# Performance work log

Hardware: AMD Instinct MI355X
Metric: run time of the kernel (lower is better)

Reference implementation:

```python
import jax, jax.numpy as jnp
from jax import lax
import numpy as np

B, C, H, W = 16, 64, 224, 224
O = 128
PH, PW = 16, 16          # patch_size (== patch_stride => non-overlapping tiling)
CH, CW = 3, 3            # compressor_size
STRIDE = (1, 1)


def setup_inputs() -> dict:
    key = jax.random.key(0)
    k_x, k_w, k_c = jax.random.split(key, 3)
    x = jax.random.normal(k_x, (B, C, H, W), dtype=jnp.float32)
    # xavier-uniform-like init scales
    pw_scale = float(np.sqrt(6.0 / (PH * PW + PH * PW)))
    patch_weight = jax.random.uniform(k_w, (C, PH, PW), jnp.float32, -pw_scale, pw_scale)
    patch_bias = jnp.zeros((C, PH, PW), jnp.float32)
    c_scale = float(np.sqrt(6.0 / (CH * CW + CH * CW)))
    compressor = jax.random.uniform(k_c, (O, CH, CW), jnp.float32, -c_scale, c_scale)
    return {"x": x, "patch_weight": patch_weight, "patch_bias": patch_bias,
            "compressor": compressor}


def _self_conv2d(x, patch_weight, patch_bias, compressor):
    b, c, h, w = x.shape
    # tile into non-overlapping patches: (B, C, nH, PH, nW, PW)
    y = x.reshape(b, c, h // PH, PH, w // PW, PW)
    # per-channel, per-intra-patch-position affine (broadcast over batch & tiles)
    y = y * patch_weight.reshape(1, c, 1, PH, 1, PW) + patch_bias.reshape(1, c, 1, PH, 1, PW)
    y = y.reshape(b, c, h, w)
    # compressor: channel-shared kernel -> (O, C, CH, CW)
    kernel = jnp.broadcast_to(compressor[:, None, :, :], (compressor.shape[0], c, CH, CW))
    out = lax.conv_general_dilated(
        y, kernel, window_strides=STRIDE, padding='VALID',
        dimension_numbers=('NCHW', 'OIHW', 'NCHW'))
    return out  # (B, O, H-CH+1, W-CW+1)


def reference(x, patch_weight, patch_bias, compressor):
    return _self_conv2d(x, patch_weight, patch_bias, compressor)
```

## Files before the change

kernel.cpp:

```cpp
#include <hip/hip_runtime.h>


#define NB 16
#define NC 64
#define NH 224
#define NW 224
#define NO 128
#define OH 222
#define OW 222

__global__ __launch_bounds__(256) void chansum_kernel(
    const float* __restrict__ x, const float* __restrict__ pw,
    const float* __restrict__ pb, float* __restrict__ s)
{
    int q   = blockIdx.x * 256 + threadIdx.x;
    int w4  = q % 56;
    int tmp = q / 56;
    int h   = tmp % NH;
    int b   = tmp / NH;
    int w0  = w4 * 4;
    int hp  = h & 15;
    int wq  = w0 & 15;

    const float4* xp  = (const float4*)(x + (((size_t)b * NC) * NH + h) * NW + w0);
    const float4* pwp = (const float4*)(pw + hp * 16 + wq);
    const float4* pbp = (const float4*)(pb + hp * 16 + wq);

    float4 acc = make_float4(0.f, 0.f, 0.f, 0.f);
    #pragma unroll 8
    for (int c = 0; c < NC; ++c) {
        float4 xv  = xp[(size_t)c * (NH * NW / 4)];
        float4 pwv = pwp[c * 64];
        float4 pbv = pbp[c * 64];
        acc.x = fmaf(xv.x, pwv.x, acc.x) + pbv.x;
        acc.y = fmaf(xv.y, pwv.y, acc.y) + pbv.y;
        acc.z = fmaf(xv.z, pwv.z, acc.z) + pbv.z;
        acc.w = fmaf(xv.w, pwv.w, acc.w) + pbv.w;
    }
    ((float4*)s)[q] = acc;
}

__global__ __launch_bounds__(128) void conv_kernel(
    const float* __restrict__ s, const float* __restrict__ comp,
    float* __restrict__ out)
{
    int bi = blockIdx.x;
    int b  = bi / OH;
    int i  = bi - b * OH;
    int jp = threadIdx.x;
    if (jp >= OW / 2) return;

    float r[3][4];
    #pragma unroll
    for (int kh = 0; kh < 3; ++kh) {
        const float2* sp = (const float2*)(s + (((size_t)b * NH) + i + kh) * NW + 2 * jp);
        float2 lo = sp[0], hi = sp[1];
        r[kh][0] = lo.x; r[kh][1] = lo.y; r[kh][2] = hi.x; r[kh][3] = hi.y;
    }

    float2* outp = (float2*)out + ((size_t)b * NO * OH + i) * (OW / 2) + jp;
    const size_t ostride = (size_t)OH * (OW / 2);

    #pragma unroll 4
    for (int o = 0; o < NO; ++o) {
        const float* cw = comp + o * 9;
        float a0 = 0.f, a1 = 0.f;
        #pragma unroll
        for (int kh = 0; kh < 3; ++kh) {
            float c0 = cw[kh * 3 + 0], c1 = cw[kh * 3 + 1], c2 = cw[kh * 3 + 2];
            a0 = fmaf(r[kh][0], c0, a0);
            a0 = fmaf(r[kh][1], c1, a0);
            a0 = fmaf(r[kh][2], c2, a0);
            a1 = fmaf(r[kh][1], c0, a1);
            a1 = fmaf(r[kh][2], c1, a1);
            a1 = fmaf(r[kh][3], c2, a1);
        }
        outp[(size_t)o * ostride] = make_float2(a0, a1);
    }
}

__global__ __launch_bounds__(128) void fused_kernel(
    const float* __restrict__ x, const float* __restrict__ pw,
    const float* __restrict__ pb, const float* __restrict__ comp,
    float* __restrict__ out)
{
    __shared__ float s[3 * NW];
    int bi = blockIdx.x;
    int b  = bi / OH;
    int i  = bi - b * OH;

    for (int p = threadIdx.x; p < 3 * NW; p += 128) {
        int rr = p / NW, w = p - rr * NW;
        int h  = i + rr;
        int hp = h & 15, wq = w & 15;
        const float* xp  = x + (((size_t)b * NC) * NH + h) * NW + w;
        const float* pwp = pw + hp * 16 + wq;
        const float* pbp = pb + hp * 16 + wq;
        float acc = 0.f;
        for (int c = 0; c < NC; ++c)
            acc = fmaf(xp[(size_t)c * NH * NW], pwp[c * 256], acc) + pbp[c * 256];
        s[p] = acc;
    }
    __syncthreads();

    int jp = threadIdx.x;
    if (jp >= OW / 2) return;

    float r[3][4];
    #pragma unroll
    for (int kh = 0; kh < 3; ++kh)
        #pragma unroll
        for (int m = 0; m < 4; ++m)
            r[kh][m] = s[kh * NW + 2 * jp + m];

    float2* outp = (float2*)out + ((size_t)b * NO * OH + i) * (OW / 2) + jp;
    const size_t ostride = (size_t)OH * (OW / 2);

    #pragma unroll 4
    for (int o = 0; o < NO; ++o) {
        const float* cw = comp + o * 9;
        float a0 = 0.f, a1 = 0.f;
        #pragma unroll
        for (int kh = 0; kh < 3; ++kh) {
            float c0 = cw[kh * 3 + 0], c1 = cw[kh * 3 + 1], c2 = cw[kh * 3 + 2];
            a0 = fmaf(r[kh][0], c0, a0);
            a0 = fmaf(r[kh][1], c1, a0);
            a0 = fmaf(r[kh][2], c2, a0);
            a1 = fmaf(r[kh][1], c0, a1);
            a1 = fmaf(r[kh][2], c1, a1);
            a1 = fmaf(r[kh][3], c2, a1);
        }
        outp[(size_t)o * ostride] = make_float2(a0, a1);
    }
}

extern "C" void kernel_launch(void* const* d_in, const int* in_sizes, int n_in,
                              void* d_out, int out_size, void* d_ws, size_t ws_size,
                              hipStream_t stream) {
    const float* x    = (const float*)d_in[0];
    const float* pw   = (const float*)d_in[1];
    const float* pb   = (const float*)d_in[2];
    const float* comp = (const float*)d_in[3];
    float* out = (float*)d_out;

    const size_t s_bytes = (size_t)NB * NH * NW * sizeof(float);
    if (ws_size >= s_bytes) {
        float* s = (float*)d_ws;
        chansum_kernel<<<(NB * NH * (NW / 4)) / 256, 256, 0, stream>>>(x, pw, pb, s);
        conv_kernel<<<NB * OH, 128, 0, stream>>>(s, comp, out);
    } else {
        fused_kernel<<<NB * OH, 128, 0, stream>>>(x, pw, pb, comp, out);
    }
}
```

Measured before the change: 588.8 us.

## Presum bias, give each thread two rows in chansum, four outputs per thread in conv

Adds a tiny kernel that sums the patch bias over channels once, so the channel-sum kernel no longer loads the bias per channel. The channel-sum kernel now has each thread process two rows 112 apart and reuse one patch-weight load for both. The conv kernel now computes four adjacent outputs per thread from a 3x6 register window and writes them with a packed 16-byte store (8-byte aligned, since the row width 222 is not a multiple of 4), with a two-wide tail at the last column. The aim is fewer weight and bias loads and wider stores, at the cost of an extra kernel launch and lower thread counts in both main kernels.

```diff
diff --git a/kernel.cpp b/kernel.cpp
--- a/kernel.cpp
+++ b/kernel.cpp
@@ -9,73 +9,119 @@
 #define OH 222
 #define OW 222
 
-__global__ __launch_bounds__(256) void chansum_kernel(
+#define S_BYTES ((size_t)NB * NH * NW * sizeof(float))
+
+struct __attribute__((packed, aligned(8))) f4u { float x, y, z, w; };
+
+__global__ __launch_bounds__(256) void biassum_kernel(
+    const float* __restrict__ pb, float* __restrict__ pbsum)
+{
+    int t = threadIdx.x;
+    float a = 0.f;
+    #pragma unroll
+    for (int c = 0; c < NC; ++c) a += pb[c * 256 + t];
+    pbsum[t] = a;
+}
+
+__global__ __launch_bounds__(128) void chansum2_kernel(
     const float* __restrict__ x, const float* __restrict__ pw,
-    const float* __restrict__ pb, float* __restrict__ s)
-{
-    int q   = blockIdx.x * 256 + threadIdx.x;
+    const float* __restrict__ pbsum, float* __restrict__ s)
+{
+    int q   = blockIdx.x * 128 + threadIdx.x;
     int w4  = q % 56;
     int tmp = q / 56;
-    int h   = tmp % NH;
-    int b   = tmp / NH;
+    int h   = tmp % 112;
+    int b   = tmp / 112;
     int w0  = w4 * 4;
     int hp  = h & 15;
     int wq  = w0 & 15;
 
-    const float4* xp  = (const float4*)(x + (((size_t)b * NC) * NH + h) * NW + w0);
+    const float4* xp0 = (const float4*)(x + (((size_t)b * NC) * NH + h) * NW + w0);
+    const float4* xp1 = xp0 + (112 * NW / 4);
     const float4* pwp = (const float4*)(pw + hp * 16 + wq);
-    const float4* pbp = (const float4*)(pb + hp * 16 + wq);
-
-    float4 acc = make_float4(0.f, 0.f, 0.f, 0.f);
+
+    float4 a0 = make_float4(0.f, 0.f, 0.f, 0.f);
+    float4 a1 = make_float4(0.f, 0.f, 0.f, 0.f);
     #pragma unroll 8
     for (int c = 0; c < NC; ++c) {
-        float4 xv  = xp[(size_t)c * (NH * NW / 4)];
-        float4 pwv = pwp[c * 64];
-        float4 pbv = pbp[c * 64];
-        acc.x = fmaf(xv.x, pwv.x, acc.x) + pbv.x;
-        acc.y = fmaf(xv.y, pwv.y, acc.y) + pbv.y;
-        acc.z = fmaf(xv.z, pwv.z, acc.z) + pbv.z;
-        acc.w = fmaf(xv.w, pwv.w, acc.w) + pbv.w;
-    }
-    ((float4*)s)[q] = acc;
-}
-
-__global__ __launch_bounds__(128) void conv_kernel(
+        float4 x0 = xp0[(size_t)c * (NH * NW / 4)];
+        float4 x1 = xp1[(size_t)c * (NH * NW / 4)];
+        float4 wv = pwp[c * 64];
+        a0.x = fmaf(x0.x, wv.x, a0.x);
+        a0.y = fmaf(x0.y, wv.y, a0.y);
+        a0.z = fmaf(x0.z, wv.z, a0.z);
+        a0.w = fmaf(x0.w, wv.w, a0.w);
+        a1.x = fmaf(x1.x, wv.x, a1.x);
+        a1.y = fmaf(x1.y, wv.y, a1.y);
+        a1.z = fmaf(x1.z, wv.z, a1.z);
+        a1.w = fmaf(x1.w, wv.w, a1.w);
+    }
+    float4 bv = *(const float4*)(pbsum + hp * 16 + wq);
+    a0.x += bv.x; a0.y += bv.y; a0.z += bv.z; a0.w += bv.w;
+    a1.x += bv.x; a1.y += bv.y; a1.z += bv.z; a1.w += bv.w;
+
+    size_t so = ((size_t)b * NH + h) * NW + w0;
+    *(float4*)(s + so)                    = a0;
+    *(float4*)(s + so + (size_t)112 * NW) = a1;
+}
+
+__global__ __launch_bounds__(128) void conv2_kernel(
     const float* __restrict__ s, const float* __restrict__ comp,
     float* __restrict__ out)
 {
     int bi = blockIdx.x;
-    int b  = bi / OH;
-    int i  = bi - b * OH;
-    int jp = threadIdx.x;
-    if (jp >= OW / 2) return;
-
-    float r[3][4];
+    int b  = bi / 111;
+    int ig = bi - b * 111;
+    int r  = threadIdx.x >> 6;
+    int jp = threadIdx.x & 63;
+    int i  = 2 * ig + r;
+    if (jp >= 56) return;
+    int j0 = jp * 4;
+
+    float rv[3][6];
     #pragma unroll
     for (int kh = 0; kh < 3; ++kh) {
-        const float2* sp = (const float2*)(s + (((size_t)b * NH) + i + kh) * NW + 2 * jp);
-        float2 lo = sp[0], hi = sp[1];
-        r[kh][0] = lo.x; r[kh][1] = lo.y; r[kh][2] = hi.x; r[kh][3] = hi.y;
-    }
-
-    float2* outp = (float2*)out + ((size_t)b * NO * OH + i) * (OW / 2) + jp;
-    const size_t ostride = (size_t)OH * (OW / 2);
+        const float* sp = s + (((size_t)b * NH) + i + kh) * NW + j0;
+        float4 v = *(const float4*)sp;
+        rv[kh][0] = v.x; rv[kh][1] = v.y; rv[kh][2] = v.z; rv[kh][3] = v.w;
+        if (jp < 55) {
+            float2 t = *(const float2*)(sp + 4);
+            rv[kh][4] = t.x; rv[kh][5] = t.y;
+        } else {
+            rv[kh][4] = 0.f; rv[kh][5] = 0.f;
+        }
+    }
+
+    float* outp = out + ((size_t)b * NO * OH + i) * OW + j0;
+    const size_t ostride = (size_t)OH * OW;
 
     #pragma unroll 4
     for (int o = 0; o < NO; ++o) {
         const float* cw = comp + o * 9;
-        float a0 = 0.f, a1 = 0.f;
+        float a0 = 0.f, a1 = 0.f, a2 = 0.f, a3 = 0.f;
         #pragma unroll
         for (int kh = 0; kh < 3; ++kh) {
             float c0 = cw[kh * 3 + 0], c1 = cw[kh * 3 + 1], c2 = cw[kh * 3 + 2];
-            a0 = fmaf(r[kh][0], c0, a0);
-            a0 = fmaf(r[kh][1], c1, a0);
-            a0 = fmaf(r[kh][2], c2, a0);
-            a1 = fmaf(r[kh][1], c0, a1);
-            a1 = fmaf(r[kh][2], c1, a1);
-            a1 = fmaf(r[kh][3], c2, a1);
-        }
-        outp[(size_t)o * ostride] = make_float2(a0, a1);
+            a0 = fmaf(rv[kh][0], c0, a0);
+            a0 = fmaf(rv[kh][1], c1, a0);
+            a0 = fmaf(rv[kh][2], c2, a0);
+            a1 = fmaf(rv[kh][1], c0, a1);
+            a1 = fmaf(rv[kh][2], c1, a1);
+            a1 = fmaf(rv[kh][3], c2, a1);
+            a2 = fmaf(rv[kh][2], c0, a2);
+            a2 = fmaf(rv[kh][3], c1, a2);
+            a2 = fmaf(rv[kh][4], c2, a2);
+            a3 = fmaf(rv[kh][3], c0, a3);
+            a3 = fmaf(rv[kh][4], c1, a3);
+            a3 = fmaf(rv[kh][5], c2, a3);
+        }
+        float* op = outp + (size_t)o * ostride;
+        if (jp < 55) {
+            f4u v; v.x = a0; v.y = a1; v.z = a2; v.w = a3;
+            *(f4u*)op = v;
+        } else {
+            *(float2*)op = make_float2(a0, a1);
+        }
     }
 }
 
@@ -106,12 +152,12 @@
     int jp = threadIdx.x;
     if (jp >= OW / 2) return;
 
-    float r[3][4];
+    float rr[3][4];
     #pragma unroll
     for (int kh = 0; kh < 3; ++kh)
         #pragma unroll
         for (int m = 0; m < 4; ++m)
-            r[kh][m] = s[kh * NW + 2 * jp + m];
+            rr[kh][m] = s[kh * NW + 2 * jp + m];
 
     float2* outp = (float2*)out + ((size_t)b * NO * OH + i) * (OW / 2) + jp;
     const size_t ostride = (size_t)OH * (OW / 2);
@@ -123,12 +169,12 @@
         #pragma unroll
         for (int kh = 0; kh < 3; ++kh) {
             float c0 = cw[kh * 3 + 0], c1 = cw[kh * 3 + 1], c2 = cw[kh * 3 + 2];
-            a0 = fmaf(r[kh][0], c0, a0);
-            a0 = fmaf(r[kh][1], c1, a0);
-            a0 = fmaf(r[kh][2], c2, a0);
-            a1 = fmaf(r[kh][1], c0, a1);
-            a1 = fmaf(r[kh][2], c1, a1);
-            a1 = fmaf(r[kh][3], c2, a1);
+            a0 = fmaf(rr[kh][0], c0, a0);
+            a0 = fmaf(rr[kh][1], c1, a0);
+            a0 = fmaf(rr[kh][2], c2, a0);
+            a1 = fmaf(rr[kh][1], c0, a1);
+            a1 = fmaf(rr[kh][2], c1, a1);
+            a1 = fmaf(rr[kh][3], c2, a1);
         }
         outp[(size_t)o * ostride] = make_float2(a0, a1);
     }
@@ -143,11 +189,12 @@
     const float* comp = (const float*)d_in[3];
     float* out = (float*)d_out;
 
-    const size_t s_bytes = (size_t)NB * NH * NW * sizeof(float);
-    if (ws_size >= s_bytes) {
-        float* s = (float*)d_ws;
-        chansum_kernel<<<(NB * NH * (NW / 4)) / 256, 256, 0, stream>>>(x, pw, pb, s);
-        conv_kernel<<<NB * OH, 128, 0, stream>>>(s, comp, out);
+    if (ws_size >= S_BYTES + 1024) {
+        float* s     = (float*)d_ws;
+        float* pbsum = (float*)((char*)d_ws + S_BYTES);
+        biassum_kernel<<<1, 256, 0, stream>>>(pb, pbsum);
+        chansum2_kernel<<<784, 128, 0, stream>>>(x, pw, pbsum, s);
+        conv2_kernel<<<NB * 111, 128, 0, stream>>>(s, comp, out);
     } else {
         fused_kernel<<<NB * OH, 128, 0, stream>>>(x, pw, pb, comp, out);
     }
```

Result: faster. 571.1 us (-3.0%).

## Fuse channel-sum and 3x3 conv into row-tiled kernel with presummed bias

Applied to the files above, without the earlier changes.

Replaces the two-pass approach (channel-sum to workspace, then conv) with one fused kernel per batch and 6-row output tile. Each block computes 8 weighted channel-sum rows into shared memory, then each wave handles a subset of output channels and writes 4 contiguous outputs per thread. The bias is summed over channels once in a tiny separate kernel, which removes per-channel bias loads. This drops the workspace round trip but recomputes two halo rows per tile, which re-reads about a third more of x.

```diff
diff --git a/kernel.cpp b/kernel.cpp
--- a/kernel.cpp
+++ b/kernel.cpp
@@ -8,129 +8,132 @@
 #define NO 128
 #define OH 222
 #define OW 222
+#define TI 6
+#define NT 37
+#define SROWS (TI + 2)
 
-__global__ __launch_bounds__(256) void chansum_kernel(
-    const float* __restrict__ x, const float* __restrict__ pw,
-    const float* __restrict__ pb, float* __restrict__ s)
+struct __attribute__((packed, aligned(8))) f4u { float x, y, z, w; };
+
+__global__ __launch_bounds__(256) void biassum_kernel(
+    const float* __restrict__ pb, float* __restrict__ pbsum)
 {
-    int q   = blockIdx.x * 256 + threadIdx.x;
-    int w4  = q % 56;
-    int tmp = q / 56;
-    int h   = tmp % NH;
-    int b   = tmp / NH;
-    int w0  = w4 * 4;
-    int hp  = h & 15;
-    int wq  = w0 & 15;
-
-    const float4* xp  = (const float4*)(x + (((size_t)b * NC) * NH + h) * NW + w0);
-    const float4* pwp = (const float4*)(pw + hp * 16 + wq);
-    const float4* pbp = (const float4*)(pb + hp * 16 + wq);
-
-    float4 acc = make_float4(0.f, 0.f, 0.f, 0.f);
-    #pragma unroll 8
-    for (int c = 0; c < NC; ++c) {
-        float4 xv  = xp[(size_t)c * (NH * NW / 4)];
-        float4 pwv = pwp[c * 64];
-        float4 pbv = pbp[c * 64];
-        acc.x = fmaf(xv.x, pwv.x, acc.x) + pbv.x;
-        acc.y = fmaf(xv.y, pwv.y, acc.y) + pbv.y;
-        acc.z = fmaf(xv.z, pwv.z, acc.z) + pbv.z;
-        acc.w = fmaf(xv.w, pwv.w, acc.w) + pbv.w;
-    }
-    ((float4*)s)[q] = acc;
+    int t = threadIdx.x;
+    float a = 0.f;
+    #pragma unroll
+    for (int c = 0; c < NC; ++c) a += pb[c * 256 + t];
+    pbsum[t] = a;
 }
 
-__global__ __launch_bounds__(128) void conv_kernel(
-    const float* __restrict__ s, const float* __restrict__ comp,
-    float* __restrict__ out)
+template<bool USE_PBSUM>
+__global__ __launch_bounds__(512) void fused6_kernel(
+    const float* __restrict__ x, const float* __restrict__ pw,
+    const float* __restrict__ pbx,
+    const float* __restrict__ comp, float* __restrict__ out)
 {
-    int bi = blockIdx.x;
-    int b  = bi / OH;
-    int i  = bi - b * OH;
-    int jp = threadIdx.x;
-    if (jp >= OW / 2) return;
+    __shared__ __align__(16) float s[SROWS * NW];
 
-    float r[3][4];
-    #pragma unroll
-    for (int kh = 0; kh < 3; ++kh) {
-        const float2* sp = (const float2*)(s + (((size_t)b * NH) + i + kh) * NW + 2 * jp);
-        float2 lo = sp[0], hi = sp[1];
-        r[kh][0] = lo.x; r[kh][1] = lo.y; r[kh][2] = hi.x; r[kh][3] = hi.y;
-    }
+    int blk = blockIdx.x;
+    int b   = blk / NT;
+    int it  = blk - b * NT;
+    int i0  = it * TI;
+    int tid = threadIdx.x;
 
-    float2* outp = (float2*)out + ((size_t)b * NO * OH + i) * (OW / 2) + jp;
-    const size_t ostride = (size_t)OH * (OW / 2);
+    if (tid < SROWS * (NW / 4)) {
+        int row = tid / (NW / 4);
+        int w4  = tid - row * (NW / 4);
+        int h   = i0 + row;
+        int w0  = 4 * w4;
+        int hp  = h & 15;
+        int wq  = w0 & 15;
 
-    #pragma unroll 4
-    for (int o = 0; o < NO; ++o) {
-        const float* cw = comp + o * 9;
-        float a0 = 0.f, a1 = 0.f;
-        #pragma unroll
-        for (int kh = 0; kh < 3; ++kh) {
-            float c0 = cw[kh * 3 + 0], c1 = cw[kh * 3 + 1], c2 = cw[kh * 3 + 2];
-            a0 = fmaf(r[kh][0], c0, a0);
-            a0 = fmaf(r[kh][1], c1, a0);
-            a0 = fmaf(r[kh][2], c2, a0);
-            a1 = fmaf(r[kh][1], c0, a1);
-            a1 = fmaf(r[kh][2], c1, a1);
-            a1 = fmaf(r[kh][3], c2, a1);
+        const float4* xp  = (const float4*)(x + (((size_t)b * NC) * NH + h) * NW + w0);
+        const float4* pwp = (const float4*)(pw + hp * 16 + wq);
+
+        float4 a = make_float4(0.f, 0.f, 0.f, 0.f);
+        if (USE_PBSUM) {
+            #pragma unroll 8
+            for (int c = 0; c < NC; ++c) {
+                float4 xv = xp[(size_t)c * (NH * NW / 4)];
+                float4 wv = pwp[c * 64];
+                a.x = fmaf(xv.x, wv.x, a.x);
+                a.y = fmaf(xv.y, wv.y, a.y);
+                a.z = fmaf(xv.z, wv.z, a.z);
+                a.w = fmaf(xv.w, wv.w, a.w);
+            }
+            float4 bv = *(const float4*)(pbx + hp * 16 + wq);
+            a.x += bv.x; a.y += bv.y; a.z += bv.z; a.w += bv.w;
+        } else {
+            const float4* pbp = (const float4*)(pbx + hp * 16 + wq);
+            #pragma unroll 8
+            for (int c = 0; c < NC; ++c) {
+                float4 xv = xp[(size_t)c * (NH * NW / 4)];
+                float4 wv = pwp[c * 64];
+                float4 bv = pbp[c * 64];
+                a.x = fmaf(xv.x, wv.x, a.x) + bv.x;
+                a.y = fmaf(xv.y, wv.y, a.y) + bv.y;
+                a.z = fmaf(xv.z, wv.z, a.z) + bv.z;
+                a.w = fmaf(xv.w, wv.w, a.w) + bv.w;
+            }
         }
-        outp[(size_t)o * ostride] = make_float2(a0, a1);
-    }
-}
-
-__global__ __launch_bounds__(128) void fused_kernel(
-    const float* __restrict__ x, const float* __restrict__ pw,
-    const float* __restrict__ pb, const float* __restrict__ comp,
-    float* __restrict__ out)
-{
-    __shared__ float s[3 * NW];
-    int bi = blockIdx.x;
-    int b  = bi / OH;
-    int i  = bi - b * OH;
-
-    for (int p = threadIdx.x; p < 3 * NW; p += 128) {
-        int rr = p / NW, w = p - rr * NW;
-        int h  = i + rr;
-        int hp = h & 15, wq = w & 15;
-        const float* xp  = x + (((size_t)b * NC) * NH + h) * NW + w;
-        const float* pwp = pw + hp * 16 + wq;
-        const float* pbp = pb + hp * 16 + wq;
-        float acc = 0.f;
-        for (int c = 0; c < NC; ++c)
-            acc = fmaf(xp[(size_t)c * NH * NW], pwp[c * 256], acc) + pbp[c * 256];
-        s[p] = acc;
+        *(float4*)(&s[row * NW + w0]) = a;
     }
     __syncthreads();
 
-    int jp = threadIdx.x;
-    if (jp >= OW / 2) return;
+    int wave = tid >> 6;
+    int jp   = tid & 63;
+    if (jp >= 56) return;
+    int j0 = 4 * jp;
 
-    float r[3][4];
+    float rv[SROWS][6];
     #pragma unroll
-    for (int kh = 0; kh < 3; ++kh)
+    for (int r = 0; r < SROWS; ++r) {
+        const float* sp = &s[r * NW + j0];
+        float4 v = *(const float4*)sp;
+        rv[r][0] = v.x; rv[r][1] = v.y; rv[r][2] = v.z; rv[r][3] = v.w;
+        if (jp < 55) {
+            float2 t = *(const float2*)(sp + 4);
+            rv[r][4] = t.x; rv[r][5] = t.y;
+        } else {
+            rv[r][4] = 0.f; rv[r][5] = 0.f;
+        }
+    }
+
+    #pragma unroll 2
+    for (int oi = 0; oi < NO / 8; ++oi) {
+        int o = wave + 8 * oi;
+        const float* cw = comp + o * 9;
+        float c00 = cw[0], c01 = cw[1], c02 = cw[2];
+        float c10 = cw[3], c11 = cw[4], c12 = cw[5];
+        float c20 = cw[6], c21 = cw[7], c22 = cw[8];
+
+        float* obase = out + (((size_t)b * NO + o) * OH + i0) * OW + j0;
         #pragma unroll
-        for (int m = 0; m < 4; ++m)
-            r[kh][m] = s[kh * NW + 2 * jp + m];
+        for (int row = 0; row < TI; ++row) {
+            const float* r0 = rv[row + 0];
+            const float* r1 = rv[row + 1];
+            const float* r2 = rv[row + 2];
+            float a0 = 0.f, a1 = 0.f, a2 = 0.f, a3 = 0.f;
+            a0 = fmaf(r0[0], c00, a0); a0 = fmaf(r0[1], c01, a0); a0 = fmaf(r0[2], c02, a0);
+            a0 = fmaf(r1[0], c10, a0); a0 = fmaf(r1[1], c11, a0); a0 = fmaf(r1[2], c12, a0);
+            a0 = fmaf(r2[0], c20, a0); a0 = fmaf(r2[1], c21, a0); a0 = fmaf(r2[2], c22, a0);
+            a1 = fmaf(r0[1], c00, a1); a1 = fmaf(r0[2], c01, a1); a1 = fmaf(r0[3], c02, a1);
+            a1 = fmaf(r1[1], c10, a1); a1 = fmaf(r1[2], c11, a1); a1 = fmaf(r1[3], c12, a1);
+            a1 = fmaf(r2[1], c20, a1); a1 = fmaf(r2[2], c21, a1); a1 = fmaf(r2[3], c22, a1);
+            a2 = fmaf(r0[2], c00, a2); a2 = fmaf(r0[3], c01, a2); a2 = fmaf(r0[4], c02, a2);
+            a2 = fmaf(r1[2], c10, a2); a2 = fmaf(r1[3], c11, a2); a2 = fmaf(r1[4], c12, a2);
+            a2 = fmaf(r2[2], c20, a2); a2 = fmaf(r2[3], c21, a2); a2 = fmaf(r2[4], c22, a2);
+            a3 = fmaf(r0[3], c00, a3); a3 = fmaf(r0[4], c01, a3); a3 = fmaf(r0[5], c02, a3);
+            a3 = fmaf(r1[3], c10, a3); a3 = fmaf(r1[4], c11, a3); a3 = fmaf(r1[5], c12, a3);
+            a3 = fmaf(r2[3], c20, a3); a3 = fmaf(r2[4], c21, a3); a3 = fmaf(r2[5], c22, a3);
 
-    float2* outp = (float2*)out + ((size_t)b * NO * OH + i) * (OW / 2) + jp;
-    const size_t ostride = (size_t)OH * (OW / 2);
-
-    #pragma unroll 4
-    for (int o = 0; o < NO; ++o) {
-        const float* cw = comp + o * 9;
-        float a0 = 0.f, a1 = 0.f;
-        #pragma unroll
-        for (int kh = 0; kh < 3; ++kh) {
-            float c0 = cw[kh * 3 + 0], c1 = cw[kh * 3 + 1], c2 = cw[kh * 3 + 2];
-            a0 = fmaf(r[kh][0], c0, a0);
-            a0 = fmaf(r[kh][1], c1, a0);
-            a0 = fmaf(r[kh][2], c2, a0);
-            a1 = fmaf(r[kh][1], c0, a1);
-            a1 = fmaf(r[kh][2], c1, a1);
-            a1 = fmaf(r[kh][3], c2, a1);
+            float* op = obase + (size_t)row * OW;
+            if (jp < 55) {
+                f4u v; v.x = a0; v.y = a1; v.z = a2; v.w = a3;
+                *(f4u*)op = v;
+            } else {
+                *(float2*)op = make_float2(a0, a1);
+            }
         }
-        outp[(size_t)o * ostride] = make_float2(a0, a1);
     }
 }
 
@@ -143,12 +146,11 @@
     const float* comp = (const float*)d_in[3];
     float* out = (float*)d_out;
 
-    const size_t s_bytes = (size_t)NB * NH * NW * sizeof(float);
-    if (ws_size >= s_bytes) {
-        float* s = (float*)d_ws;
-        chansum_kernel<<<(NB * NH * (NW / 4)) / 256, 256, 0, stream>>>(x, pw, pb, s);
-        conv_kernel<<<NB * OH, 128, 0, stream>>>(s, comp, out);
+    if (ws_size >= 1024) {
+        float* pbsum = (float*)d_ws;
+        biassum_kernel<<<1, 256, 0, stream>>>(pb, pbsum);
+        fused6_kernel<true><<<NB * NT, 512, 0, stream>>>(x, pw, pbsum, comp, out);
     } else {
-        fused_kernel<<<NB * OH, 128, 0, stream>>>(x, pw, pb, comp, out);
+        fused6_kernel<false><<<NB * NT, 512, 0, stream>>>(x, pw, pb, comp, out);
     }
 }
```

Measured after the change: 561.4 us. 4.7% less time.
